# Kernel optimization log

Hardware: AMD Instinct MI355X
Metric: run time of the kernel (lower is better)

Reference implementation:

```python
import jax, jax.numpy as jnp
import numpy as np
from jax import lax

B, C, H, W = 16, 128, 128, 128
WS, K = 2, 7
EPS = 1e-5


def setup_inputs() -> dict:
    key = jax.random.key(0)
    ks = jax.random.split(key, 4)
    s = 0.02
    return {
        "x": jax.random.normal(ks[0], (B, C, H, W), jnp.float32),
        "bn_gamma": jnp.ones((C,), jnp.float32),
        "bn_beta": jnp.zeros((C,), jnp.float32),
        "bn_mean": jnp.zeros((C,), jnp.float32),
        "bn_var": jnp.ones((C,), jnp.float32),
        "dw_w": jax.random.normal(ks[1], (C, 1, K, K), jnp.float32) * s,  # depthwise OIHW, groups=C
        "dw_b": jnp.zeros((C,), jnp.float32),
        "qkv_w": jax.random.normal(ks[2], (3 * C, C), jnp.float32) * s,  # 1x1 conv weight
        "qkv_b": jnp.zeros((3 * C,), jnp.float32),
        "proj_w": jax.random.normal(ks[3], (C, C), jnp.float32) * s,
        "proj_b": jnp.zeros((C,), jnp.float32),
    }


def reference(x, bn_gamma, bn_beta, bn_mean, bn_var, dw_w, dw_b, qkv_w, qkv_b, proj_w, proj_b):
    b, c, h, w = x.shape
    h2, w2 = h // WS, w // WS
    L = h2 * w2
    # --- ggm: BatchNorm (eval) -> GELU -> depthwise conv k=7 stride=2 pad=3 ---
    inv = lax.rsqrt(bn_var + EPS)
    xn = (x - bn_mean[None, :, None, None]) * (bn_gamma * inv)[None, :, None, None] + bn_beta[None, :, None, None]
    g = jax.nn.gelu(xn, approximate=False)
    guide = lax.conv_general_dilated(
        g, dw_w, window_strides=(WS, WS), padding=[(K // 2, K // 2), (K // 2, K // 2)],
        feature_group_count=c, dimension_numbers=("NCHW", "OIHW", "NCHW"),
    ) + dw_b[None, :, None, None]  # [B,C,H2,W2]
    # --- unfold(kernel=2, stride=2): non-overlapping 2x2 windows -> [B,C,4,L] ---
    xu = x.reshape(b, c, h2, WS, w2, WS).transpose(0, 1, 3, 5, 2, 4).reshape(b, c, WS * WS, L)
    tokens = jnp.concatenate([guide.reshape(b, c, 1, L), xu], axis=2)  # [B,C,5,L]
    # --- qkv 1x1 conv ---
    qkv = jnp.einsum("bcnl,dc->bdnl", tokens, qkv_w) + qkv_b[None, :, None, None]
    q, k, v = jnp.split(qkv, 3, axis=1)  # each [B,C,5,L]
    # --- tiny 5x5 attention per channel, contracting over the L window axis ---
    attn = jnp.einsum("bcnl,bcml->bcnm", q, k) / jnp.sqrt(jnp.float32(c))
    attn = jax.nn.softmax(attn, axis=-1)
    out = jnp.einsum("bcnm,bcml->bcnl", attn, v)  # [B,C,5,L]
    # take the guide-token row and fold back to the window grid
    out0 = out[:, :, 0, :].reshape(b, c, h2, w2)
    return jnp.einsum("bchw,dc->bdhw", out0, proj_w) + proj_b[None, :, None, None]
```

## Files before the change

kernel.cpp:

```cpp
#include <hip/hip_runtime.h>
#include <math.h>

#define BB 16
#define CC 128
#define HH 128
#define WW 128
#define LL 4096

typedef short short8 __attribute__((ext_vector_type(8)));
typedef float f32x4 __attribute__((ext_vector_type(4)));

__device__ __forceinline__ ushort f2bf(float f) {
    union { float f; unsigned u; } un; un.f = f;
    unsigned u = un.u;
    u += 0x7fffu + ((u >> 16) & 1u);
    return (ushort)(u >> 16);
}
__device__ __forceinline__ float bf2f(ushort h) {
    union { unsigned u; float f; } un; un.u = ((unsigned)h) << 16;
    return un.f;
}
__device__ __forceinline__ float fast_gelu(float xv) {
    float x2 = xv*xv;
    float arg = xv*(-2.3022100f - 0.1029436f*x2);
    float e = exp2f(arg);
    return xv*__builtin_amdgcn_rcpf(1.f + e);
}
__device__ __forceinline__ int swzkey(int r) { return (r & 3) ^ ((r >> 2) & 3); }

__global__ __launch_bounds__(128) void prep_cvec(
    const float* __restrict__ qkv_b, const float* __restrict__ proj_w,
    const float* __restrict__ proj_b, float* __restrict__ cvec)
{
    int t = threadIdx.x;
    float s = proj_b[t];
    const float* pr = proj_w + t*CC;
    const float* bv = qkv_b + 2*CC;
    for (int c = 0; c < CC; ++c) s += pr[c]*bv[c];
    cvec[t] = s;
}

__global__ __launch_bounds__(256) void guide_kernel(
    const float* __restrict__ x, const float* __restrict__ gamma,
    const float* __restrict__ beta, const float* __restrict__ mean,
    const float* __restrict__ var, const float* __restrict__ dww,
    const float* __restrict__ dwb, ushort* __restrict__ gw)
{
    int bc = blockIdx.x;
    int b = bc >> 7, c = bc & 127;
    int ty = blockIdx.y;
    __shared__ __align__(16) float g[69*144];
    int t = threadIdx.x;
    float wreg[49];
    #pragma unroll
    for (int k = 0; k < 49; ++k) wreg[k] = dww[c*49 + k];
    float bias = dwb[c];
    float scl = gamma[c] * rsqrtf(var[c] + 1e-5f);
    float sft = beta[c] - mean[c]*scl;
    const float* xb = x + (size_t)(b*CC + c)*HH*WW;
    int ihbase = 64*ty - 3;
    #pragma unroll
    for (int k = 0; k < 9; ++k) {
        int idx = k*256 + t;
        if (idx < 69*32) {
            int row = idx >> 5, ch = idx & 31;
            int ih = ihbase + row;
            float4 v4 = {0.f, 0.f, 0.f, 0.f};
            if ((unsigned)ih < 128u) {
                float4 xv = *(const float4*)(xb + ih*WW + 4*ch);
                v4.x = fast_gelu(xv.x*scl + sft);
                v4.y = fast_gelu(xv.y*scl + sft);
                v4.z = fast_gelu(xv.z*scl + sft);
                v4.w = fast_gelu(xv.w*scl + sft);
            }
            int f = (row >> 2) & 3;
            *(float4*)(g + row*144 + 4*((ch + 1) ^ f)) = v4;
        }
    }
    if (t < 138) {
        int row = t >> 1;
        int lc = (t & 1) ? 33 : 0;
        int f = (row >> 2) & 3;
        float4 z4 = {0.f, 0.f, 0.f, 0.f};
        *(float4*)(g + row*144 + 4*(lc ^ f)) = z4;
    }
    __syncthreads();
    int vg = t >> 4, owg = t & 15;
    float acc[2][4];
    #pragma unroll
    for (int v = 0; v < 2; ++v)
        #pragma unroll
        for (int hh = 0; hh < 4; ++hh) acc[v][hh] = bias;
    #pragma unroll
    for (int j = 0; j < 9; ++j) {
        int rr = 4*vg + j;
        int f = (rr >> 2) & 3;
        const float* grow = g + rr*144;
        float win[16];
        #pragma unroll
        for (int i = 0; i < 4; ++i) {
            float4 w4 = *(const float4*)(grow + 4*(((2*owg + i) ^ f)));
            win[4*i+0] = w4.x; win[4*i+1] = w4.y;
            win[4*i+2] = w4.z; win[4*i+3] = w4.w;
        }
        #pragma unroll
        for (int v = 0; v < 2; ++v) {
            int kh = j - 2*v;
            if (kh >= 0 && kh <= 6) {
                #pragma unroll
                for (int hh = 0; hh < 4; ++hh)
                    #pragma unroll
                    for (int kw = 0; kw < 7; ++kw)
                        acc[v][hh] += wreg[kh*7 + kw] * win[2*hh + kw + 1];
            }
        }
    }
    int orbase = 32*ty + 2*vg;
    ushort* gdst = gw + ((size_t)(b*CC + c) << 12);
    #pragma unroll
    for (int v = 0; v < 2; ++v) {
        uint2 pk;
        pk.x = (unsigned)f2bf(acc[v][0]) | ((unsigned)f2bf(acc[v][1]) << 16);
        pk.y = (unsigned)f2bf(acc[v][2]) | ((unsigned)f2bf(acc[v][3]) << 16);
        *(uint2*)(gdst + (orbase + v)*64 + 4*owg) = pk;
    }
}

__global__ __launch_bounds__(512) void gram_kernel(
    const float* __restrict__ x, const ushort* __restrict__ gw,
    ushort* __restrict__ Gpart, float* __restrict__ Tg, float* __restrict__ Txg)
{
    __shared__ __align__(16) ushort tokb[2*3*128*32];
    int t = threadIdx.x;
    int blk = blockIdx.x;
    int b = blk >> 5, kq = (blk >> 1) & 15, grp = blk & 1;
    int lane = t & 63, wid = t >> 6;
    int l15 = lane & 15, kg = lane >> 4;
    int js = t >> 2, sub = t & 3;
    int keyj = swzkey(js);
    const float* xrow0 = x + ((size_t)(b*CC + js)*HH + grp)*WW;
    const ushort* gwrow = gw + ((size_t)(b*CC + js) << 12);
    f32x4 acc[8][3];
    #pragma unroll
    for (int i = 0; i < 8; ++i)
        #pragma unroll
        for (int q = 0; q < 3; ++q) acc[i][q] = (f32x4){0.f,0.f,0.f,0.f};
    float tacc = 0.f, ps0 = 0.f, ps1 = 0.f;
    int H0 = kq*4;
    float4 xa, xbv, xc, xd;
    uint4 gr;
    {
        const float* xp = xrow0 + (2*H0)*WW + sub*16;
        xa = *(const float4*)(xp);
        xbv = *(const float4*)(xp + 4);
        xc = *(const float4*)(xp + 8);
        xd = *(const float4*)(xp + 12);
        gr = *(const uint4*)(gwrow + H0*64 + sub*8);
    }
    for (int s = 0; s < 8; ++s) {
        int cur = s & 1;
        ushort* tb = tokb + cur*(3*128*32);
        if (grp == 0) {
            tacc += bf2f((ushort)gr.x) + bf2f((ushort)(gr.x >> 16))
                  + bf2f((ushort)gr.y) + bf2f((ushort)(gr.y >> 16))
                  + bf2f((ushort)gr.z) + bf2f((ushort)(gr.z >> 16))
                  + bf2f((ushort)gr.w) + bf2f((ushort)(gr.w >> 16));
        }
        ps0 += xa.x + xa.z + xbv.x + xbv.z + xc.x + xc.z + xd.x + xd.z;
        ps1 += xa.y + xa.w + xbv.y + xbv.w + xc.y + xc.w + xd.y + xd.w;
        {
            unsigned lo0 = (unsigned)f2bf(xa.x) | ((unsigned)f2bf(xa.z) << 16);
            unsigned lo1 = (unsigned)f2bf(xbv.x) | ((unsigned)f2bf(xbv.z) << 16);
            unsigned lo2 = (unsigned)f2bf(xc.x) | ((unsigned)f2bf(xc.z) << 16);
            unsigned lo3 = (unsigned)f2bf(xd.x) | ((unsigned)f2bf(xd.z) << 16);
            unsigned hi0 = (unsigned)f2bf(xa.y) | ((unsigned)f2bf(xa.w) << 16);
            unsigned hi1 = (unsigned)f2bf(xbv.y) | ((unsigned)f2bf(xbv.w) << 16);
            unsigned hi2 = (unsigned)f2bf(xc.y) | ((unsigned)f2bf(xc.w) << 16);
            unsigned hi3 = (unsigned)f2bf(xd.y) | ((unsigned)f2bf(xd.w) << 16);
            uint4 lov = {lo0, lo1, lo2, lo3};
            uint4 hiv = {hi0, hi1, hi2, hi3};
            int chs = (sub ^ keyj) << 3;
            *(uint4*)(tb + (1*128 + js)*32 + chs) = lov;
            *(uint4*)(tb + (2*128 + js)*32 + chs) = hiv;
            *(uint4*)(tb + (0*128 + js)*32 + chs) = gr;
        }
        if (s < 7) {
            int sn = s + 1;
            int h = H0 + (sn >> 1), whalf = sn & 1;
            const float* xp = xrow0 + (2*h)*WW + whalf*64 + sub*16;
            xa = *(const float4*)(xp);
            xbv = *(const float4*)(xp + 4);
            xc = *(const float4*)(xp + 8);
            xd = *(const float4*)(xp + 12);
            gr = *(const uint4*)(gwrow + h*64 + whalf*32 + sub*8);
        }
        __syncthreads();
        const ushort* tb2 = tokb + cur*(3*128*32);
        short8 af[8];
        #pragma unroll
        for (int f = 0; f < 8; ++f) {
            int row = f*16 + l15;
            af[f] = *(const short8*)(tb2 + row*32 + ((kg ^ swzkey(row)) << 3));
        }
        if (grp == 0) {
            #pragma unroll
            for (int q = 0; q < 3; ++q) {
                int nf = wid*3 + q;
                int pl = nf >> 3, jr = (nf & 7)*16 + l15;
                short8 bf = *(const short8*)(tb2 + (pl*128 + jr)*32 + ((kg ^ swzkey(jr)) << 3));
                #pragma unroll
                for (int f = 0; f < 8; ++f)
                    acc[f][q] = __builtin_amdgcn_mfma_f32_16x16x32_bf16(af[f], bf, acc[f][q], 0, 0, 0);
            }
        } else {
            #pragma unroll
            for (int q = 0; q < 2; ++q) {
                int nf = wid*2 + q;
                int pl = 1 + (nf >> 3), jr = (nf & 7)*16 + l15;
                short8 bf = *(const short8*)(tb2 + (pl*128 + jr)*32 + ((kg ^ swzkey(jr)) << 3));
                #pragma unroll
                for (int f = 0; f < 8; ++f)
                    acc[f][q] = __builtin_amdgcn_mfma_f32_16x16x32_bf16(af[f], bf, acc[f][q], 0, 0, 0);
            }
        }
    }
    ps0 += __shfl_xor(ps0, 1); ps0 += __shfl_xor(ps0, 2);
    ps1 += __shfl_xor(ps1, 1); ps1 += __shfl_xor(ps1, 2);
    if (grp == 0) {
        tacc += __shfl_xor(tacc, 1); tacc += __shfl_xor(tacc, 2);
        if (sub == 0) Tg[(size_t)(b*16 + kq)*128 + js] = tacc;
    }
    if (sub == 0) {
        float* tx = Txg + (((size_t)(b*16 + kq)*2 + grp)*2)*128;
        tx[js] = ps0;
        tx[128 + js] = ps1;
    }
    ushort* gp = Gpart + (size_t)(b*16 + kq)*81920;
    int nq = (grp == 0) ? 3 : 2;
    int nbase = (grp == 0) ? 0 : 384;
    #pragma unroll
    for (int f = 0; f < 8; ++f)
        #pragma unroll
        for (int q = 0; q < 3; ++q) {
            if (q < nq) {
                int n = nbase + (wid*nq + q)*16 + l15;
                uint2 pk;
                pk.x = (unsigned)f2bf(acc[f][q][0]) | ((unsigned)f2bf(acc[f][q][1]) << 16);
                pk.y = (unsigned)f2bf(acc[f][q][2]) | ((unsigned)f2bf(acc[f][q][3]) << 16);
                *(uint2*)(gp + ((size_t)(f*4 + kg)*640 + n)*4) = pk;
            }
        }
}

__global__ __launch_bounds__(256) void combine2_kernel(
    const ushort* __restrict__ Gpart, const float* __restrict__ qkv_w,
    float* __restrict__ Spart2)
{
    __shared__ float Gm[32*128];
    int blk = blockIdx.x;
    int iq = blk & 3, bm = blk >> 2;
    int b = bm / 5, m = bm - b*5;
    int t = threadIdx.x;
    for (int e = t; e < 1024; e += 256) {
        int qi = e >> 7, j = e & 127;
        float s0=0.f, s1=0.f, s2=0.f, s3=0.f;
        #pragma unroll
        for (int kq = 0; kq < 16; ++kq) {
            uint2 v = *(const uint2*)(Gpart + (size_t)(b*16 + kq)*81920
                        + ((size_t)(iq*8 + qi)*640 + m*128 + j)*4);
            s0 += bf2f((ushort)v.x); s1 += bf2f((ushort)(v.x >> 16));
            s2 += bf2f((ushort)v.y); s3 += bf2f((ushort)(v.y >> 16));
        }
        Gm[(qi*4 + 0)*128 + j] = s0;
        Gm[(qi*4 + 1)*128 + j] = s1;
        Gm[(qi*4 + 2)*128 + j] = s2;
        Gm[(qi*4 + 3)*128 + j] = s3;
    }
    __syncthreads();
    int c = t >> 1, jh = t & 1;
    float wkr[64];
    const float* wkp = qkv_w + (size_t)(128 + c)*128 + jh*64;
    #pragma unroll
    for (int q = 0; q < 16; ++q)
        *(float4*)&wkr[q*4] = ((const float4*)wkp)[q];
    const float* wqp = qkv_w + (size_t)c*128 + iq*32;
    float acc = 0.f;
    for (int i = 0; i < 32; ++i) {
        const float4* gr4 = (const float4*)(Gm + i*128 + jh*64);
        float val = 0.f;
        #pragma unroll
        for (int q = 0; q < 16; ++q) {
            float4 g4 = gr4[q];
            val += wkr[q*4+0]*g4.x + wkr[q*4+1]*g4.y
                 + wkr[q*4+2]*g4.z + wkr[q*4+3]*g4.w;
        }
        acc += wqp[i]*val;
    }
    acc += __shfl_xor(acc, 1);
    if (jh == 0) Spart2[((size_t)bm*4 + iq)*128 + c] = acc;
}

__global__ __launch_bounds__(128) void softmax_attn(
    const float* __restrict__ Spart2, const float* __restrict__ Tg,
    const float* __restrict__ Txg, const float* __restrict__ qkv_w,
    const float* __restrict__ qkv_b, float* __restrict__ attn)
{
    __shared__ float Ts[5*128];
    int b = blockIdx.x, t = threadIdx.x;
    #pragma unroll
    for (int v = 0; v < 5; ++v) {
        float s = 0.f;
        if (v == 0) {
            for (int p = 0; p < 16; ++p) s += Tg[(size_t)(b*16 + p)*128 + t];
        } else {
            int grp = (v - 1) >> 1, pi = (v - 1) & 1;
            for (int p = 0; p < 16; ++p)
                s += Txg[(((size_t)(b*16 + p)*2 + grp)*2 + pi)*128 + t];
        }
        Ts[v*128 + t] = s;
    }
    __syncthreads();
    int c = t;
    float bq = qkv_b[c], bk = qkv_b[128 + c];
    const float* wqr = qkv_w + (size_t)c*128;
    const float* wkr = qkv_w + (size_t)(128 + c)*128;
    float t0d = 0.f;
    for (int j = 0; j < 128; ++j) t0d += wqr[j]*Ts[j];
    float s5[5];
    #pragma unroll
    for (int m = 0; m < 5; ++m) {
        float km = 0.f;
        for (int j = 0; j < 128; ++j) km += wkr[j]*Ts[m*128 + j];
        float ss = 0.f;
        #pragma unroll
        for (int iq = 0; iq < 4; ++iq)
            ss += Spart2[((size_t)(b*5 + m)*4 + iq)*128 + c];
        s5[m] = ss + bq*km + bk*t0d + 4096.0f*bq*bk;
    }
    const float scale = 0.08838834764831845f;
    float mx = s5[0]*scale;
    #pragma unroll
    for (int m = 1; m < 5; ++m) mx = fmaxf(mx, s5[m]*scale);
    float e[5], tot = 0.f;
    #pragma unroll
    for (int m = 0; m < 5; ++m) { e[m] = expf(s5[m]*scale - mx); tot += e[m]; }
    float inv = 1.f/tot;
    #pragma unroll
    for (int m = 0; m < 5; ++m) attn[(size_t)(b*128 + c)*5 + m] = e[m]*inv;
}

__global__ __launch_bounds__(256) void pw_kernel(
    const float* __restrict__ qkv_w, const float* __restrict__ proj_w,
    const float* __restrict__ attn, ushort* __restrict__ PW)
{
    __shared__ float attns[CC];
    __shared__ float wvs[32*CC];
    int blk = blockIdx.x;
    int b = blk / 5, m = blk % 5;
    int t = threadIdx.x;
    if (t < CC) attns[t] = attn[(b*CC + t)*5 + m];
    int d = t >> 1, cb = (t & 1)*64;
    float acc[64];
    #pragma unroll
    for (int j = 0; j < 64; ++j) acc[j] = 0.f;
    for (int cc0 = 0; cc0 < CC; cc0 += 32) {
        __syncthreads();
        for (int idx = t; idx < 32*CC; idx += 256) {
            int row = idx >> 7, col = idx & 127;
            wvs[idx] = qkv_w[(2*CC + cc0 + row)*CC + col];
        }
        __syncthreads();
        for (int cl = 0; cl < 32; ++cl) {
            int c = cc0 + cl;
            float a = proj_w[d*CC + c]*attns[c];
            const float* wr = wvs + cl*CC + cb;
            #pragma unroll
            for (int j = 0; j < 64; ++j) acc[j] += a*wr[j];
        }
    }
    ushort* dst = PW + ((size_t)(b*5 + m) << 14) + d*CC + cb;
    #pragma unroll
    for (int j = 0; j < 64; ++j) dst[j] = f2bf(acc[j]);
}

__global__ __launch_bounds__(256) void y_kernel(
    const float* __restrict__ x, const ushort* __restrict__ gw,
    const ushort* __restrict__ PW, const float* __restrict__ cvec,
    float* __restrict__ out)
{
    __shared__ __align__(16) ushort tok[5*32*128];
    int t = threadIdx.x;
    int blk = blockIdx.x;
    int b = blk >> 7, chunk = blk & 127;
    int h = chunk >> 1, whalf = chunk & 1;
    int lane = t & 63, wave = t >> 6;
    int l15 = lane & 15, kg = lane >> 4;
    int swz = (l15 & 7) << 3;
    int c = t >> 1, r = t & 1;
    const ushort* gsrc = gw + ((size_t)(b*CC + c) << 12) + h*64 + whalf*32 + r*16;
    uint4 g0 = *(const uint4*)gsrc;
    uint4 g1 = *(const uint4*)(gsrc + 8);
    const float* xrow = x + ((size_t)(b*CC + c)*HH + 2*h + r)*WW + whalf*64;
    float4 xv[16];
    #pragma unroll
    for (int i = 0; i < 16; ++i) xv[i] = ((const float4*)xrow)[i];
    {
        unsigned wd[8] = {g0.x,g0.y,g0.z,g0.w,g1.x,g1.y,g1.z,g1.w};
        #pragma unroll
        for (int k2 = 0; k2 < 8; ++k2) {
            int lp0 = r*16 + 2*k2, lp1 = lp0 + 1;
            tok[lp0*128 + (c ^ ((lp0 & 7) << 3))] = (ushort)wd[k2];
            tok[lp1*128 + (c ^ ((lp1 & 7) << 3))] = (ushort)(wd[k2] >> 16);
        }
    }
    {
        int mA = (1 + 2*r)*4096, mB = (2 + 2*r)*4096;
        #pragma unroll
        for (int i = 0; i < 16; ++i) {
            int lp0 = 2*i, lp1 = 2*i + 1;
            int o0 = lp0*128 + (c ^ ((lp0 & 7) << 3));
            int o1 = lp1*128 + (c ^ ((lp1 & 7) << 3));
            tok[mA + o0] = f2bf(xv[i].x);
            tok[mB + o0] = f2bf(xv[i].y);
            tok[mA + o1] = f2bf(xv[i].z);
            tok[mB + o1] = f2bf(xv[i].w);
        }
    }
    __syncthreads();
    f32x4 acc[2][2] = {};
    #pragma unroll
    for (int m = 0; m < 5; ++m) {
        const ushort* pwb = PW + ((size_t)(b*5 + m) << 14)
                          + ((wave*32 + l15) << 7) + (kg << 3);
        #pragma unroll
        for (int kt = 0; kt < 4; ++kt) {
            int ko = (kt*32 + kg*8) ^ swz;
            short8 a0 = *(const short8*)(tok + m*4096 + (l15     )*128 + ko);
            short8 a1 = *(const short8*)(tok + m*4096 + (16 + l15)*128 + ko);
            short8 b0 = *(const short8*)(pwb + kt*32);
            short8 b1 = *(const short8*)(pwb + (16 << 7) + kt*32);
            acc[0][0] = __builtin_amdgcn_mfma_f32_16x16x32_bf16(a0, b0, acc[0][0], 0, 0, 0);
            acc[0][1] = __builtin_amdgcn_mfma_f32_16x16x32_bf16(a0, b1, acc[0][1], 0, 0, 0);
            acc[1][0] = __builtin_amdgcn_mfma_f32_16x16x32_bf16(a1, b0, acc[1][0], 0, 0, 0);
            acc[1][1] = __builtin_amdgcn_mfma_f32_16x16x32_bf16(a1, b1, acc[1][1], 0, 0, 0);
        }
    }
    __syncthreads();
    float* ylds = (float*)tok;
    #pragma unroll
    for (int mt = 0; mt < 2; ++mt)
        #pragma unroll
        for (int ntl = 0; ntl < 2; ++ntl) {
            int cc = wave*32 + ntl*16 + l15;
            float cv = cvec[cc];
            #pragma unroll
            for (int rr = 0; rr < 4; ++rr) {
                int l = mt*16 + kg*4 + rr;
                ylds[cc*36 + l] = acc[mt][ntl][rr] + cv;
            }
        }
    __syncthreads();
    int c2 = t >> 1, half = t & 1;
    float* ob = out + ((size_t)(b*CC + c2) << 12) + h*64 + whalf*32 + half*16;
    const float* yr = ylds + c2*36 + half*16;
    #pragma unroll
    for (int j = 0; j < 4; ++j)
        ((float4*)ob)[j] = ((const float4*)yr)[j];
}

extern "C" void kernel_launch(void* const* d_in, const int* in_sizes, int n_in,
                              void* d_out, int out_size, void* d_ws, size_t ws_size,
                              hipStream_t stream) {
    const float* x        = (const float*)d_in[0];
    const float* bn_gamma = (const float*)d_in[1];
    const float* bn_beta  = (const float*)d_in[2];
    const float* bn_mean  = (const float*)d_in[3];
    const float* bn_var   = (const float*)d_in[4];
    const float* dw_w     = (const float*)d_in[5];
    const float* dw_b     = (const float*)d_in[6];
    const float* qkv_w    = (const float*)d_in[7];
    const float* qkv_b    = (const float*)d_in[8];
    const float* proj_w   = (const float*)d_in[9];
    const float* proj_b   = (const float*)d_in[10];
    float* out = (float*)d_out;

    char* w = (char*)d_ws;
    ushort* gw     = (ushort*)w; w += (size_t)BB*CC*LL*2;
    ushort* PW     = (ushort*)w; w += (size_t)BB*5*CC*CC*2;
    ushort* Gpart  = (ushort*)w; w += (size_t)BB*16*81920*2;
    float*  Tg     = (float*)w;  w += (size_t)BB*16*128*4;
    float*  Txg    = (float*)w;  w += (size_t)BB*16*2*2*128*4;
    float*  Spart2 = (float*)w;  w += (size_t)BB*5*4*128*4;
    float*  attn   = (float*)w;  w += (size_t)BB*CC*5*4;
    float*  cvec   = (float*)w;  w += (size_t)CC*4;

    prep_cvec<<<1, 128, 0, stream>>>(qkv_b, proj_w, proj_b, cvec);
    guide_kernel<<<dim3(BB*CC, 2), 256, 0, stream>>>(
        x, bn_gamma, bn_beta, bn_mean, bn_var, dw_w, dw_b, gw);
    gram_kernel<<<512, 512, 0, stream>>>(x, gw, Gpart, Tg, Txg);
    combine2_kernel<<<BB*5*4, 256, 0, stream>>>(Gpart, qkv_w, Spart2);
    softmax_attn<<<BB, 128, 0, stream>>>(Spart2, Tg, Txg, qkv_w, qkv_b, attn);
    pw_kernel<<<BB*5, 256, 0, stream>>>(qkv_w, proj_w, attn, PW);
    y_kernel<<<2048, 256, 0, stream>>>(x, gw, PW, cvec, out);
}
```

Baseline: 222.1 us.

## Fuse softmax into pw_kernel and widen y_kernel to full rows

The per-batch softmax attention kernel is folded into pw_kernel. Each block now recomputes the token sums and the softmax for its batch and keeps only the column it needs, which removes one launch and the attn buffer round-trip. Each pw block redoes the softmax work, five times per batch in total. Separately, y_kernel now processes a full 64-wide row per block with 512 threads and twice the LDS. This halves the block count, allows each PW tile load to be reused across more tokens, and lowers occupancy per CU.

```diff
diff --git a/kernel.cpp b/kernel.cpp
--- a/kernel.cpp
+++ b/kernel.cpp
@@ -300,65 +300,58 @@
     if (jh == 0) Spart2[((size_t)bm*4 + iq)*128 + c] = acc;
 }
 
-__global__ __launch_bounds__(128) void softmax_attn(
+__global__ __launch_bounds__(256) void pw_kernel(
     const float* __restrict__ Spart2, const float* __restrict__ Tg,
     const float* __restrict__ Txg, const float* __restrict__ qkv_w,
-    const float* __restrict__ qkv_b, float* __restrict__ attn)
-{
+    const float* __restrict__ qkv_b, const float* __restrict__ proj_w,
+    ushort* __restrict__ PW)
+{
+    __shared__ float attns[CC];
     __shared__ float Ts[5*128];
-    int b = blockIdx.x, t = threadIdx.x;
-    #pragma unroll
-    for (int v = 0; v < 5; ++v) {
+    __shared__ float wvs[32*CC];
+    int blk = blockIdx.x;
+    int b = blk / 5, m = blk % 5;
+    int t = threadIdx.x;
+    for (int i = t; i < 640; i += 256) {
+        int v = i >> 7, cch = i & 127;
         float s = 0.f;
         if (v == 0) {
-            for (int p = 0; p < 16; ++p) s += Tg[(size_t)(b*16 + p)*128 + t];
+            for (int p = 0; p < 16; ++p) s += Tg[(size_t)(b*16 + p)*128 + cch];
         } else {
             int grp = (v - 1) >> 1, pi = (v - 1) & 1;
             for (int p = 0; p < 16; ++p)
-                s += Txg[(((size_t)(b*16 + p)*2 + grp)*2 + pi)*128 + t];
-        }
-        Ts[v*128 + t] = s;
-    }
-    __syncthreads();
-    int c = t;
-    float bq = qkv_b[c], bk = qkv_b[128 + c];
-    const float* wqr = qkv_w + (size_t)c*128;
-    const float* wkr = qkv_w + (size_t)(128 + c)*128;
-    float t0d = 0.f;
-    for (int j = 0; j < 128; ++j) t0d += wqr[j]*Ts[j];
-    float s5[5];
-    #pragma unroll
-    for (int m = 0; m < 5; ++m) {
-        float km = 0.f;
-        for (int j = 0; j < 128; ++j) km += wkr[j]*Ts[m*128 + j];
-        float ss = 0.f;
-        #pragma unroll
-        for (int iq = 0; iq < 4; ++iq)
-            ss += Spart2[((size_t)(b*5 + m)*4 + iq)*128 + c];
-        s5[m] = ss + bq*km + bk*t0d + 4096.0f*bq*bk;
-    }
-    const float scale = 0.08838834764831845f;
-    float mx = s5[0]*scale;
-    #pragma unroll
-    for (int m = 1; m < 5; ++m) mx = fmaxf(mx, s5[m]*scale);
-    float e[5], tot = 0.f;
-    #pragma unroll
-    for (int m = 0; m < 5; ++m) { e[m] = expf(s5[m]*scale - mx); tot += e[m]; }
-    float inv = 1.f/tot;
-    #pragma unroll
-    for (int m = 0; m < 5; ++m) attn[(size_t)(b*128 + c)*5 + m] = e[m]*inv;
-}
-
-__global__ __launch_bounds__(256) void pw_kernel(
-    const float* __restrict__ qkv_w, const float* __restrict__ proj_w,
-    const float* __restrict__ attn, ushort* __restrict__ PW)
-{
-    __shared__ float attns[CC];
-    __shared__ float wvs[32*CC];
-    int blk = blockIdx.x;
-    int b = blk / 5, m = blk % 5;
-    int t = threadIdx.x;
-    if (t < CC) attns[t] = attn[(b*CC + t)*5 + m];
+                s += Txg[(((size_t)(b*16 + p)*2 + grp)*2 + pi)*128 + cch];
+        }
+        Ts[v*128 + cch] = s;
+    }
+    __syncthreads();
+    if (t < 128) {
+        int cc = t;
+        float bq = qkv_b[cc], bk = qkv_b[128 + cc];
+        const float* wqr = qkv_w + (size_t)cc*128;
+        const float* wkr = qkv_w + (size_t)(128 + cc)*128;
+        float t0d = 0.f;
+        for (int j = 0; j < 128; ++j) t0d += wqr[j]*Ts[j];
+        float s5[5];
+        #pragma unroll
+        for (int mm = 0; mm < 5; ++mm) {
+            float km = 0.f;
+            for (int j = 0; j < 128; ++j) km += wkr[j]*Ts[mm*128 + j];
+            float ss = 0.f;
+            #pragma unroll
+            for (int iq = 0; iq < 4; ++iq)
+                ss += Spart2[((size_t)(b*5 + mm)*4 + iq)*128 + cc];
+            s5[mm] = ss + bq*km + bk*t0d + 4096.0f*bq*bk;
+        }
+        const float scale = 0.08838834764831845f;
+        float mx = s5[0]*scale;
+        #pragma unroll
+        for (int mm = 1; mm < 5; ++mm) mx = fmaxf(mx, s5[mm]*scale);
+        float e[5], tot = 0.f;
+        #pragma unroll
+        for (int mm = 0; mm < 5; ++mm) { e[mm] = expf(s5[mm]*scale - mx); tot += e[mm]; }
+        attns[cc] = e[m]/tot;
+    }
     int d = t >> 1, cb = (t & 1)*64;
     float acc[64];
     #pragma unroll
@@ -383,24 +376,26 @@
     for (int j = 0; j < 64; ++j) dst[j] = f2bf(acc[j]);
 }
 
-__global__ __launch_bounds__(256) void y_kernel(
+__global__ __launch_bounds__(512) void y_kernel(
     const float* __restrict__ x, const ushort* __restrict__ gw,
     const ushort* __restrict__ PW, const float* __restrict__ cvec,
     float* __restrict__ out)
 {
-    __shared__ __align__(16) ushort tok[5*32*128];
+    __shared__ __align__(16) ushort tok[5*64*128];
     int t = threadIdx.x;
     int blk = blockIdx.x;
-    int b = blk >> 7, chunk = blk & 127;
-    int h = chunk >> 1, whalf = chunk & 1;
+    int b = blk >> 6, h = blk & 63;
     int lane = t & 63, wave = t >> 6;
     int l15 = lane & 15, kg = lane >> 4;
     int swz = (l15 & 7) << 3;
-    int c = t >> 1, r = t & 1;
-    const ushort* gsrc = gw + ((size_t)(b*CC + c) << 12) + h*64 + whalf*32 + r*16;
+    int lbase = (wave >> 2)*32;
+    int cq = (wave & 3)*32;
+    int c = t >> 2, r2 = t & 3;
+    int r = r2 >> 1, half = r2 & 1;
+    const ushort* gsrc = gw + ((size_t)(b*CC + c) << 12) + h*64 + r2*16;
     uint4 g0 = *(const uint4*)gsrc;
     uint4 g1 = *(const uint4*)(gsrc + 8);
-    const float* xrow = x + ((size_t)(b*CC + c)*HH + 2*h + r)*WW + whalf*64;
+    const float* xrow = x + ((size_t)(b*CC + c)*HH + 2*h + r)*WW + half*64;
     float4 xv[16];
     #pragma unroll
     for (int i = 0; i < 16; ++i) xv[i] = ((const float4*)xrow)[i];
@@ -408,16 +403,17 @@
         unsigned wd[8] = {g0.x,g0.y,g0.z,g0.w,g1.x,g1.y,g1.z,g1.w};
         #pragma unroll
         for (int k2 = 0; k2 < 8; ++k2) {
-            int lp0 = r*16 + 2*k2, lp1 = lp0 + 1;
+            int lp0 = r2*16 + 2*k2, lp1 = lp0 + 1;
             tok[lp0*128 + (c ^ ((lp0 & 7) << 3))] = (ushort)wd[k2];
             tok[lp1*128 + (c ^ ((lp1 & 7) << 3))] = (ushort)(wd[k2] >> 16);
         }
     }
     {
-        int mA = (1 + 2*r)*4096, mB = (2 + 2*r)*4096;
+        int mA = (1 + 2*r)*8192, mB = (2 + 2*r)*8192;
+        int lb = half*32;
         #pragma unroll
         for (int i = 0; i < 16; ++i) {
-            int lp0 = 2*i, lp1 = 2*i + 1;
+            int lp0 = lb + 2*i, lp1 = lp0 + 1;
             int o0 = lp0*128 + (c ^ ((lp0 & 7) << 3));
             int o1 = lp1*128 + (c ^ ((lp1 & 7) << 3));
             tok[mA + o0] = f2bf(xv[i].x);
@@ -431,12 +427,12 @@
     #pragma unroll
     for (int m = 0; m < 5; ++m) {
         const ushort* pwb = PW + ((size_t)(b*5 + m) << 14)
-                          + ((wave*32 + l15) << 7) + (kg << 3);
+                          + ((cq + l15) << 7) + (kg << 3);
         #pragma unroll
         for (int kt = 0; kt < 4; ++kt) {
             int ko = (kt*32 + kg*8) ^ swz;
-            short8 a0 = *(const short8*)(tok + m*4096 + (l15     )*128 + ko);
-            short8 a1 = *(const short8*)(tok + m*4096 + (16 + l15)*128 + ko);
+            short8 a0 = *(const short8*)(tok + m*8192 + (lbase + l15     )*128 + ko);
+            short8 a1 = *(const short8*)(tok + m*8192 + (lbase + 16 + l15)*128 + ko);
             short8 b0 = *(const short8*)(pwb + kt*32);
             short8 b1 = *(const short8*)(pwb + (16 << 7) + kt*32);
             acc[0][0] = __builtin_amdgcn_mfma_f32_16x16x32_bf16(a0, b0, acc[0][0], 0, 0, 0);
@@ -451,18 +447,18 @@
     for (int mt = 0; mt < 2; ++mt)
         #pragma unroll
         for (int ntl = 0; ntl < 2; ++ntl) {
-            int cc = wave*32 + ntl*16 + l15;
+            int cc = cq + ntl*16 + l15;
             float cv = cvec[cc];
             #pragma unroll
             for (int rr = 0; rr < 4; ++rr) {
-                int l = mt*16 + kg*4 + rr;
-                ylds[cc*36 + l] = acc[mt][ntl][rr] + cv;
-            }
-        }
-    __syncthreads();
-    int c2 = t >> 1, half = t & 1;
-    float* ob = out + ((size_t)(b*CC + c2) << 12) + h*64 + whalf*32 + half*16;
-    const float* yr = ylds + c2*36 + half*16;
+                int l = lbase + mt*16 + kg*4 + rr;
+                ylds[cc*68 + l] = acc[mt][ntl][rr] + cv;
+            }
+        }
+    __syncthreads();
+    int c2 = t >> 2, q = t & 3;
+    float* ob = out + ((size_t)(b*CC + c2) << 12) + h*64 + q*16;
+    const float* yr = ylds + c2*68 + q*16;
     #pragma unroll
     for (int j = 0; j < 4; ++j)
         ((float4*)ob)[j] = ((const float4*)yr)[j];
@@ -491,7 +487,6 @@
     float*  Tg     = (float*)w;  w += (size_t)BB*16*128*4;
     float*  Txg    = (float*)w;  w += (size_t)BB*16*2*2*128*4;
     float*  Spart2 = (float*)w;  w += (size_t)BB*5*4*128*4;
-    float*  attn   = (float*)w;  w += (size_t)BB*CC*5*4;
     float*  cvec   = (float*)w;  w += (size_t)CC*4;
 
     prep_cvec<<<1, 128, 0, stream>>>(qkv_b, proj_w, proj_b, cvec);
@@ -499,7 +494,6 @@
         x, bn_gamma, bn_beta, bn_mean, bn_var, dw_w, dw_b, gw);
     gram_kernel<<<512, 512, 0, stream>>>(x, gw, Gpart, Tg, Txg);
     combine2_kernel<<<BB*5*4, 256, 0, stream>>>(Gpart, qkv_w, Spart2);
-    softmax_attn<<<BB, 128, 0, stream>>>(Spart2, Tg, Txg, qkv_w, qkv_b, attn);
-    pw_kernel<<<BB*5, 256, 0, stream>>>(qkv_w, proj_w, attn, PW);
-    y_kernel<<<2048, 256, 0, stream>>>(x, gw, PW, cvec, out);
-}
+    pw_kernel<<<BB*5, 256, 0, stream>>>(Spart2, Tg, Txg, qkv_w, qkv_b, proj_w, PW);
+    y_kernel<<<BB*64, 512, 0, stream>>>(x, gw, PW, cvec, out);
+}
```

Result: slower. 246.2 us (+10.9%).

## Split pw_kernel over output column quarters and widen y_kernel to full rows

Applied to the files above, without the earlier changes.

pw_kernel now runs 4x more blocks, each computing a 32-column slice with the full qkv_w V-slice loaded once into padded shared memory. This cuts per-thread accumulators from 64 to 16 and raises parallelism for a launch that had only 80 blocks. y_kernel now processes a full output row pair per block with 512 threads and double the LDS tile, halving the block count. The larger LDS footprint may reduce occupancy.

```diff
diff --git a/kernel.cpp b/kernel.cpp
--- a/kernel.cpp
+++ b/kernel.cpp
@@ -354,53 +354,53 @@
     const float* __restrict__ attn, ushort* __restrict__ PW)
 {
     __shared__ float attns[CC];
-    __shared__ float wvs[32*CC];
+    __shared__ float wvs[128*33];
     int blk = blockIdx.x;
-    int b = blk / 5, m = blk % 5;
+    int jq = blk & 3, bm = blk >> 2;
+    int b = bm / 5, m = bm - b*5;
     int t = threadIdx.x;
-    if (t < CC) attns[t] = attn[(b*CC + t)*5 + m];
-    int d = t >> 1, cb = (t & 1)*64;
-    float acc[64];
-    #pragma unroll
-    for (int j = 0; j < 64; ++j) acc[j] = 0.f;
-    for (int cc0 = 0; cc0 < CC; cc0 += 32) {
-        __syncthreads();
-        for (int idx = t; idx < 32*CC; idx += 256) {
-            int row = idx >> 7, col = idx & 127;
-            wvs[idx] = qkv_w[(2*CC + cc0 + row)*CC + col];
-        }
-        __syncthreads();
-        for (int cl = 0; cl < 32; ++cl) {
-            int c = cc0 + cl;
-            float a = proj_w[d*CC + c]*attns[c];
-            const float* wr = wvs + cl*CC + cb;
-            #pragma unroll
-            for (int j = 0; j < 64; ++j) acc[j] += a*wr[j];
-        }
-    }
-    ushort* dst = PW + ((size_t)(b*5 + m) << 14) + d*CC + cb;
-    #pragma unroll
-    for (int j = 0; j < 64; ++j) dst[j] = f2bf(acc[j]);
-}
-
-__global__ __launch_bounds__(256) void y_kernel(
+    if (t < 128) attns[t] = attn[(size_t)(b*CC + t)*5 + m];
+    for (int idx = t; idx < 128*32; idx += 256) {
+        int row = idx >> 5, col = idx & 31;
+        wvs[row*33 + col] = qkv_w[(size_t)(2*CC + row)*CC + jq*32 + col];
+    }
+    __syncthreads();
+    int d = t >> 1, jh = t & 1;
+    float acc[16];
+    #pragma unroll
+    for (int j = 0; j < 16; ++j) acc[j] = 0.f;
+    const float* pr = proj_w + (size_t)d*CC;
+    for (int c = 0; c < 128; ++c) {
+        float a = pr[c]*attns[c];
+        const float* wr = wvs + c*33 + jh*16;
+        #pragma unroll
+        for (int j = 0; j < 16; ++j) acc[j] += a*wr[j];
+    }
+    ushort* dst = PW + ((size_t)(b*5 + m) << 14) + (size_t)d*CC + jq*32 + jh*16;
+    #pragma unroll
+    for (int j = 0; j < 16; ++j) dst[j] = f2bf(acc[j]);
+}
+
+__global__ __launch_bounds__(512) void y_kernel(
     const float* __restrict__ x, const ushort* __restrict__ gw,
     const ushort* __restrict__ PW, const float* __restrict__ cvec,
     float* __restrict__ out)
 {
-    __shared__ __align__(16) ushort tok[5*32*128];
+    __shared__ __align__(16) ushort tok[5*64*128];
     int t = threadIdx.x;
     int blk = blockIdx.x;
-    int b = blk >> 7, chunk = blk & 127;
-    int h = chunk >> 1, whalf = chunk & 1;
+    int b = blk >> 6, h = blk & 63;
     int lane = t & 63, wave = t >> 6;
     int l15 = lane & 15, kg = lane >> 4;
     int swz = (l15 & 7) << 3;
-    int c = t >> 1, r = t & 1;
-    const ushort* gsrc = gw + ((size_t)(b*CC + c) << 12) + h*64 + whalf*32 + r*16;
+    int lbase = (wave >> 2)*32;
+    int cq = (wave & 3)*32;
+    int c = t >> 2, r2 = t & 3;
+    int r = r2 >> 1, half = r2 & 1;
+    const ushort* gsrc = gw + ((size_t)(b*CC + c) << 12) + h*64 + r2*16;
     uint4 g0 = *(const uint4*)gsrc;
     uint4 g1 = *(const uint4*)(gsrc + 8);
-    const float* xrow = x + ((size_t)(b*CC + c)*HH + 2*h + r)*WW + whalf*64;
+    const float* xrow = x + ((size_t)(b*CC + c)*HH + 2*h + r)*WW + half*64;
     float4 xv[16];
     #pragma unroll
     for (int i = 0; i < 16; ++i) xv[i] = ((const float4*)xrow)[i];
@@ -408,16 +408,17 @@
         unsigned wd[8] = {g0.x,g0.y,g0.z,g0.w,g1.x,g1.y,g1.z,g1.w};
         #pragma unroll
         for (int k2 = 0; k2 < 8; ++k2) {
-            int lp0 = r*16 + 2*k2, lp1 = lp0 + 1;
+            int lp0 = r2*16 + 2*k2, lp1 = lp0 + 1;
             tok[lp0*128 + (c ^ ((lp0 & 7) << 3))] = (ushort)wd[k2];
             tok[lp1*128 + (c ^ ((lp1 & 7) << 3))] = (ushort)(wd[k2] >> 16);
         }
     }
     {
-        int mA = (1 + 2*r)*4096, mB = (2 + 2*r)*4096;
+        int mA = (1 + 2*r)*8192, mB = (2 + 2*r)*8192;
+        int lb = half*32;
         #pragma unroll
         for (int i = 0; i < 16; ++i) {
-            int lp0 = 2*i, lp1 = 2*i + 1;
+            int lp0 = lb + 2*i, lp1 = lp0 + 1;
             int o0 = lp0*128 + (c ^ ((lp0 & 7) << 3));
             int o1 = lp1*128 + (c ^ ((lp1 & 7) << 3));
             tok[mA + o0] = f2bf(xv[i].x);
@@ -431,12 +432,12 @@
     #pragma unroll
     for (int m = 0; m < 5; ++m) {
         const ushort* pwb = PW + ((size_t)(b*5 + m) << 14)
-                          + ((wave*32 + l15) << 7) + (kg << 3);
+                          + ((cq + l15) << 7) + (kg << 3);
         #pragma unroll
         for (int kt = 0; kt < 4; ++kt) {
             int ko = (kt*32 + kg*8) ^ swz;
-            short8 a0 = *(const short8*)(tok + m*4096 + (l15     )*128 + ko);
-            short8 a1 = *(const short8*)(tok + m*4096 + (16 + l15)*128 + ko);
+            short8 a0 = *(const short8*)(tok + m*8192 + (lbase + l15     )*128 + ko);
+            short8 a1 = *(const short8*)(tok + m*8192 + (lbase + 16 + l15)*128 + ko);
             short8 b0 = *(const short8*)(pwb + kt*32);
             short8 b1 = *(const short8*)(pwb + (16 << 7) + kt*32);
             acc[0][0] = __builtin_amdgcn_mfma_f32_16x16x32_bf16(a0, b0, acc[0][0], 0, 0, 0);
@@ -451,18 +452,18 @@
     for (int mt = 0; mt < 2; ++mt)
         #pragma unroll
         for (int ntl = 0; ntl < 2; ++ntl) {
-            int cc = wave*32 + ntl*16 + l15;
+            int cc = cq + ntl*16 + l15;
             float cv = cvec[cc];
             #pragma unroll
             for (int rr = 0; rr < 4; ++rr) {
-                int l = mt*16 + kg*4 + rr;
-                ylds[cc*36 + l] = acc[mt][ntl][rr] + cv;
+                int l = lbase + mt*16 + kg*4 + rr;
+                ylds[cc*68 + l] = acc[mt][ntl][rr] + cv;
             }
         }
     __syncthreads();
-    int c2 = t >> 1, half = t & 1;
-    float* ob = out + ((size_t)(b*CC + c2) << 12) + h*64 + whalf*32 + half*16;
-    const float* yr = ylds + c2*36 + half*16;
+    int c2 = t >> 2, q = t & 3;
+    float* ob = out + ((size_t)(b*CC + c2) << 12) + h*64 + q*16;
+    const float* yr = ylds + c2*68 + q*16;
     #pragma unroll
     for (int j = 0; j < 4; ++j)
         ((float4*)ob)[j] = ((const float4*)yr)[j];
@@ -500,6 +501,6 @@
     gram_kernel<<<512, 512, 0, stream>>>(x, gw, Gpart, Tg, Txg);
     combine2_kernel<<<BB*5*4, 256, 0, stream>>>(Gpart, qkv_w, Spart2);
     softmax_attn<<<BB, 128, 0, stream>>>(Spart2, Tg, Txg, qkv_w, qkv_b, attn);
-    pw_kernel<<<BB*5, 256, 0, stream>>>(qkv_w, proj_w, attn, PW);
-    y_kernel<<<2048, 256, 0, stream>>>(x, gw, PW, cvec, out);
-}
+    pw_kernel<<<BB*5*4, 256, 0, stream>>>(qkv_w, proj_w, attn, PW);
+    y_kernel<<<BB*64, 512, 0, stream>>>(x, gw, PW, cvec, out);
+}
```

Result: faster. 195.6 us (-11.9%).
